# Optimization experiments

Hardware: AMD Instinct MI355X
Metric: run time of the kernel (lower is better)

Reference implementation:

```python
import jax, jax.numpy as jnp
import numpy as np

N, E, G, D, L, T = 50000, 100000, 2000, 300, 5, 10
NUM_ATOM, NUM_CHIR, NUM_BOND, NUM_DIR = 120, 3, 6, 3


def setup_inputs() -> dict:
    key = jax.random.key(0)
    ks = jax.random.split(key, 24)
    s = 1.0 / np.sqrt(D)
    inp = {
        'x': jnp.stack([jax.random.randint(ks[0], (N,), 0, NUM_ATOM),
                        jax.random.randint(ks[1], (N,), 0, NUM_CHIR)], axis=1),
        'edge_index': jax.random.randint(ks[2], (2, E), 0, N),
        'edge_attr': jnp.stack([jax.random.randint(ks[3], (E,), 0, 4),
                                jax.random.randint(ks[4], (E,), 0, NUM_DIR)], axis=1),
        'batch': jnp.sort(jax.random.randint(ks[5], (N,), 0, G)),
        'x1': jnp.stack([jax.random.randint(ks[6], (N,), 0, NUM_ATOM),
                         jax.random.randint(ks[7], (N,), 0, NUM_CHIR)], axis=1),
        'edge_index1': jax.random.randint(ks[8], (2, E), 0, N),
        'edge_attr1': jnp.stack([jax.random.randint(ks[9], (E,), 0, 4),
                                 jax.random.randint(ks[10], (E,), 0, NUM_DIR)], axis=1),
        'batch1': jnp.sort(jax.random.randint(ks[11], (N,), 0, G)),
        'xemb1': jax.random.normal(ks[12], (NUM_ATOM, D)) * s,
        'xemb2': jax.random.normal(ks[13], (NUM_CHIR, D)) * s,
        'eemb1': jax.random.normal(ks[14], (L, NUM_BOND, D)) * s,
        'eemb2': jax.random.normal(ks[15], (L, NUM_DIR, D)) * s,
        'W1': jax.random.normal(ks[16], (L, D, 2 * D)) * s,
        'b1': jnp.zeros((L, 2 * D)),
        'W2': jax.random.normal(ks[17], (L, 2 * D, D)) * (1.0 / np.sqrt(2 * D)),
        'b2': jnp.zeros((L, D)),
        'gamma': jnp.ones((L, D)),
        'beta': jnp.zeros((L, D)),
        'predW': jax.random.normal(ks[18], (D, T)) * s,
        'predb': jnp.zeros((T,)),
    }
    return inp


def _gnn(xi, ei, ea, xemb1, xemb2, eemb1, eemb2, W1, b1, W2, b2, gamma, beta):
    n = xi.shape[0]
    h = xemb1[xi[:, 0]] + xemb2[xi[:, 1]]  # [N, D]
    loop = jnp.arange(n)
    src = jnp.concatenate([ei[0], loop])
    dst = jnp.concatenate([ei[1], loop])
    # self-loop edge attr = [4, 0]
    sl = jnp.concatenate([jnp.full((n, 1), 4, ea.dtype), jnp.zeros((n, 1), ea.dtype)], axis=1)
    eaf = jnp.concatenate([ea, sl], axis=0)
    for l in range(L):
        eemb = eemb1[l][eaf[:, 0]] + eemb2[l][eaf[:, 1]]     # [E+N, D]
        msg = h[src] + eemb                                   # gather
        agg = jax.ops.segment_sum(msg, dst, num_segments=n)   # scatter-add
        h2 = jax.nn.relu(agg @ W1[l] + b1[l]) @ W2[l] + b2[l] # GIN MLP
        mu = h2.mean(axis=0)
        var = ((h2 - mu) ** 2).mean(axis=0)                   # batchnorm (train stats)
        h2 = gamma[l] * (h2 - mu) * jax.lax.rsqrt(var + 1e-5) + beta[l]
        if l < L - 1:
            h2 = jax.nn.relu(h2)
        h = h2
    return h  # JK='last'


def _mean_pool(node_rep, batch):
    s = jax.ops.segment_sum(node_rep, batch, num_segments=G)
    cnt = jax.ops.segment_sum(jnp.ones((node_rep.shape[0],), node_rep.dtype), batch, num_segments=G)
    return s / jnp.maximum(cnt, 1.0)[:, None]


def reference(x, edge_index, edge_attr, batch, x1, edge_index1, edge_attr1, batch1,
              xemb1, xemb2, eemb1, eemb2, W1, b1, W2, b2, gamma, beta, predW, predb):
    node_rep = _gnn(x, edge_index, edge_attr, xemb1, xemb2, eemb1, eemb2, W1, b1, W2, b2, gamma, beta)
    node_rep1 = _gnn(x1, edge_index1, edge_attr1, xemb1, xemb2, eemb1, eemb2, W1, b1, W2, b2, gamma, beta)
    graph_rep = _mean_pool(node_rep, batch)
    graph_rep1 = _mean_pool(node_rep1, batch1)
    pred = graph_rep @ predW + predb
    pred1 = graph_rep1 @ predW + predb
    return (pred, graph_rep, node_rep, pred1, graph_rep1, node_rep1)
```

## Files before the change

kernel.cpp:

```cpp
#include <hip/hip_runtime.h>
#include <hip/hip_bf16.h>

typedef unsigned short ushort_t;
typedef short v8s __attribute__((ext_vector_type(8)));
typedef unsigned short v8u __attribute__((ext_vector_type(8)));
typedef unsigned short v4u __attribute__((ext_vector_type(4)));
typedef float v4f __attribute__((ext_vector_type(4)));

#define N_NODES 50000
#define N_EDGES 100000
#define N_GRAPH 2000
#define DIM     300
#define DIM2    600
#define NLAYER  5
#define NTASK   10
#define D4      75
#define D4P     80

#define LDA  304
#define NPAD 50048
#define KST1 10
#define KST2 19

#define KB1 40
#define NT1 5
#define KB2 76
#define NT2 3
#define MT_TILES 391

#define AS1 __attribute__((address_space(1)))
#define AS3 __attribute__((address_space(3)))
static __device__ __forceinline__ void gload_lds16(const void* g, void* l) {
    __builtin_amdgcn_global_load_lds((AS1 void*)(g), (AS3 void*)(l), 16, 0, 0);
}

static __device__ __forceinline__ ushort_t f2bf(float f) {
    unsigned int u;
    __builtin_memcpy(&u, &f, 4);
    unsigned int lsb = (u >> 16) & 1u;
    u += 0x7fffu + lsb;
    return (ushort_t)(u >> 16);
}
static __device__ __forceinline__ void split2(float f, ushort_t& h, ushort_t& l) {
    unsigned int u;
    __builtin_memcpy(&u, &f, 4);
    h = (ushort_t)(u >> 16);
    unsigned int um = u & 0xFFFF0000u;
    float hf;
    __builtin_memcpy(&hf, &um, 4);
    float lf = f - hf;
    unsigned int ul;
    __builtin_memcpy(&ul, &lf, 4);
    l = (ushort_t)(ul >> 16);
}

static __device__ __forceinline__ int swz_wgid(int orig, int nwg) {
    int xcd = orig & 7;
    int seq = orig >> 3;
    int q = nwg >> 3, r = nwg & 7;
    int base = (xcd < r) ? xcd * (q + 1) : r * (q + 1) + (xcd - r) * q;
    return base + seq;
}

__global__ void k_embed_init(const int* __restrict__ x,
                             const float* __restrict__ xe1,
                             const float* __restrict__ xe2,
                             float* __restrict__ h) {
    int tid = blockIdx.x * blockDim.x + threadIdx.x;
    if (tid >= N_NODES * D4) return;
    int node = tid / D4;
    int d0 = (tid % D4) * 4;
    int i0 = x[node * 2 + 0];
    int i1 = x[node * 2 + 1];
    float4 a = *(const float4*)(xe1 + (size_t)i0 * DIM + d0);
    float4 b = *(const float4*)(xe2 + (size_t)i1 * DIM + d0);
    float4 o;
    o.x = a.x + b.x; o.y = a.y + b.y; o.z = a.z + b.z; o.w = a.w + b.w;
    *(float4*)(h + (size_t)node * LDA + d0) = o;
}

__global__ void k_deg(const int* __restrict__ ei, int* __restrict__ deg) {
    int e = blockIdx.x * blockDim.x + threadIdx.x;
    if (e >= N_EDGES) return;
    atomicAdd(&deg[ei[N_EDGES + e]], 1);
}

__global__ void k_scan1(const int* __restrict__ deg, int* __restrict__ excl,
                        int* __restrict__ blksum) {
    __shared__ int s[256];
    int i = blockIdx.x * 256 + threadIdx.x;
    int v = (i < N_NODES) ? deg[i] : 0;
    s[threadIdx.x] = v;
    __syncthreads();
#pragma unroll
    for (int o = 1; o < 256; o <<= 1) {
        int t = (threadIdx.x >= o) ? s[threadIdx.x - o] : 0;
        __syncthreads();
        s[threadIdx.x] += t;
        __syncthreads();
    }
    if (i < N_NODES) excl[i] = s[threadIdx.x] - v;
    if (threadIdx.x == 255) blksum[blockIdx.x] = s[255];
}

__global__ void k_scan2(int* __restrict__ blksum, int* __restrict__ blkoff, int nblk) {
    __shared__ int s[256];
    int v = (threadIdx.x < nblk) ? blksum[threadIdx.x] : 0;
    s[threadIdx.x] = v;
    __syncthreads();
#pragma unroll
    for (int o = 1; o < 256; o <<= 1) {
        int t = (threadIdx.x >= o) ? s[threadIdx.x - o] : 0;
        __syncthreads();
        s[threadIdx.x] += t;
        __syncthreads();
    }
    if (threadIdx.x < nblk) blkoff[threadIdx.x] = s[threadIdx.x] - v;
}

__global__ void k_scan3(const int* __restrict__ excl, const int* __restrict__ blkoff,
                        int* __restrict__ rowptr, int* __restrict__ fillptr) {
    int i = blockIdx.x * blockDim.x + threadIdx.x;
    if (i > N_NODES) return;
    int v = (i < N_NODES) ? (excl[i] + blkoff[i >> 8]) : N_EDGES;
    rowptr[i] = v;
    if (i < N_NODES) fillptr[i] = v;
}

__global__ void k_fill(const int* __restrict__ ei, const int* __restrict__ ea,
                       int* __restrict__ fillptr,
                       int* __restrict__ csrc, int* __restrict__ cea) {
    int e = blockIdx.x * blockDim.x + threadIdx.x;
    if (e >= N_EDGES) return;
    int dst = ei[N_EDGES + e];
    int pos = atomicAdd(&fillptr[dst], 1);
    csrc[pos] = ei[e];
    cea[pos] = (ea[2 * e + 0] << 16) | ea[2 * e + 1];
}

template <bool BN>
__global__ void k_gather_agg(const int* __restrict__ rowptr,
                             const int* __restrict__ csrc,
                             const int* __restrict__ cea,
                             const float* __restrict__ hin,
                             const float* __restrict__ ee1,
                             const float* __restrict__ ee2,
                             const float* __restrict__ ee1sl,
                             const float* __restrict__ ee2sl,
                             const float* __restrict__ bnmean,
                             const float* __restrict__ bnrstd,
                             const float* __restrict__ bngam,
                             const float* __restrict__ bnbet,
                             ushort_t* __restrict__ aghi,
                             ushort_t* __restrict__ aglo) {
    int tid = blockIdx.x * blockDim.x + threadIdx.x;
    if (tid >= N_NODES * D4P) return;
    int node = tid / D4P;
    int c = tid % D4P;
    int d0 = c * 4;
    const int mt = node >> 7, m = node & 127;
    const int ks = d0 >> 5, kb = (d0 >> 3) & 3, jq = d0 & 7;
    const size_t off = (((size_t)mt * KST1 + ks) * 4 + kb) * 1024 + m * 8 + jq;
    if (c >= D4) {
        v4u z = (v4u){0, 0, 0, 0};
        *(v4u*)(aghi + off) = z;
        *(v4u*)(aglo + off) = z;
        return;
    }
    float4 m4, r4, g4, b4;
    if (BN) {
        m4 = *(const float4*)(bnmean + d0);
        r4 = *(const float4*)(bnrstd + d0);
        g4 = *(const float4*)(bngam + d0);
        b4 = *(const float4*)(bnbet + d0);
    }
    auto bn4 = [&](float4 v) -> float4 {
        if (BN) {
            v.x = fmaxf((v.x - m4.x) * r4.x * g4.x + b4.x, 0.f);
            v.y = fmaxf((v.y - m4.y) * r4.y * g4.y + b4.y, 0.f);
            v.z = fmaxf((v.z - m4.z) * r4.z * g4.z + b4.z, 0.f);
            v.w = fmaxf((v.w - m4.w) * r4.w * g4.w + b4.w, 0.f);
        }
        return v;
    };
    float4 a = bn4(*(const float4*)(hin + (size_t)node * LDA + d0));
    float4 e1 = *(const float4*)(ee1sl + d0);
    float4 e2 = *(const float4*)(ee2sl + d0);
    a.x += e1.x + e2.x; a.y += e1.y + e2.y; a.z += e1.z + e2.z; a.w += e1.w + e2.w;
    int p0 = rowptr[node], p1 = rowptr[node + 1];
    for (int p = p0; p < p1; ++p) {
        int src = csrc[p];
        int pk = cea[p];
        int a0 = pk >> 16, a1 = pk & 0xFFFF;
        float4 hv = bn4(*(const float4*)(hin + (size_t)src * LDA + d0));
        float4 f1 = *(const float4*)(ee1 + (size_t)a0 * DIM + d0);
        float4 f2 = *(const float4*)(ee2 + (size_t)a1 * DIM + d0);
        a.x += hv.x + f1.x + f2.x;
        a.y += hv.y + f1.y + f2.y;
        a.z += hv.z + f1.z + f2.z;
        a.w += hv.w + f1.w + f2.w;
    }
    float av[4] = {a.x, a.y, a.z, a.w};
    v4u hh, ll;
#pragma unroll
    for (int i = 0; i < 4; ++i) {
        ushort_t uh, ul;
        split2(av[i], uh, ul);
        hh[i] = uh;
        ll[i] = ul;
    }
    *(v4u*)(aghi + off) = hh;
    *(v4u*)(aglo + off) = ll;
}

__global__ void k_pack_w(const float* __restrict__ W,
                         ushort_t* __restrict__ hi,
                         ushort_t* __restrict__ lo,
                         int K, int N, int KBv, int NTv, int total) {
    int idx = blockIdx.x * blockDim.x + threadIdx.x;
    if (idx >= total) return;
    int j = idx & 7;
    int n = (idx >> 3) & 127;
    int tmp = idx >> 10;
    int kb = tmp % KBv; tmp /= KBv;
    int nt = tmp % NTv;
    int l = tmp / NTv;
    int k = kb * 8 + j;
    int ng = nt * 128 + n;
    float v = 0.f;
    if (k < K && ng < N) v = W[((size_t)l * K + k) * N + ng];
    ushort_t h, lw;
    split2(v, h, lw);
    hi[idx] = h;
    lo[idx] = lw;
}

template <bool RELU, bool SPLITA, bool BNSTAT, typename OT>
__global__ __launch_bounds__(256) void k_gemm_mfma(
        const ushort_t* __restrict__ Ahi,
        const ushort_t* __restrict__ Alo,
        const ushort_t* __restrict__ Bhi,
        const ushort_t* __restrict__ Blo,
        const float* __restrict__ bias,
        OT* __restrict__ C,
        double* __restrict__ bnsum,
        double* __restrict__ bnsq,
        int M, int N, int Ksteps, int KBv, int NTv, int nwg,
        int ldc, int ncap, int ksout) {
    alignas(16) __shared__ ushort_t sBhi[8192];
    alignas(16) __shared__ ushort_t sBlo[8192];

    const int wgid = swz_wgid(blockIdx.x, nwg);
    const int nt = wgid % NTv;
    const int mt = wgid / NTv;
    const int t = threadIdx.x;

    const int w = t >> 6;
    const int lane = t & 63;
    const int wm = w >> 1;
    const int wn = w & 1;
    const int quad = lane >> 4;
    const int lr = lane & 15;

    v4f acc[4][4];
#pragma unroll
    for (int i = 0; i < 4; ++i)
#pragma unroll
        for (int j = 0; j < 4; ++j) acc[i][j] = (v4f){0.f, 0.f, 0.f, 0.f};

    const int aoff = quad * 1024 + (wm * 64 + lr) * 8;

    auto stageB = [&](int buf, int ks) {
        const int bo = buf * 4096;
        const size_t bbase = ((size_t)nt * KBv + ks * 4) * 1024;
#pragma unroll
        for (int p = 0; p < 2; ++p) {
            int o = p * 2048 + t * 8;
            gload_lds16(Bhi + bbase + o, &sBhi[bo + o]);
            gload_lds16(Blo + bbase + o, &sBlo[bo + o]);
        }
    };

    stageB(0, 0);
    __syncthreads();
    int cur = 0;
    for (int ks = 0; ks < Ksteps; ++ks) {
        const ushort_t* ah = Ahi + ((size_t)mt * Ksteps + ks) * 4096 + aoff;
        const ushort_t* al = SPLITA ? (Alo + ((size_t)mt * Ksteps + ks) * 4096 + aoff) : nullptr;
        v8s a_hi[4], a_lo[4];
#pragma unroll
        for (int s = 0; s < 4; ++s) {
            a_hi[s] = *(const v8s*)(ah + s * 128);
            if (SPLITA) a_lo[s] = *(const v8s*)(al + s * 128);
        }
        __builtin_amdgcn_sched_barrier(0);
        if (ks + 1 < Ksteps) stageB(cur ^ 1, ks + 1);
        const int bo = cur * 4096;
#pragma unroll
        for (int sj = 0; sj < 4; ++sj) {
            v8s bh = *(const v8s*)&sBhi[bo + quad * 1024 + (wn * 64 + sj * 16 + lr) * 8];
            v8s bl = *(const v8s*)&sBlo[bo + quad * 1024 + (wn * 64 + sj * 16 + lr) * 8];
#pragma unroll
            for (int si = 0; si < 4; ++si) {
                acc[si][sj] = __builtin_amdgcn_mfma_f32_16x16x32_bf16(
                    a_hi[si], bh, acc[si][sj], 0, 0, 0);
                acc[si][sj] = __builtin_amdgcn_mfma_f32_16x16x32_bf16(
                    a_hi[si], bl, acc[si][sj], 0, 0, 0);
                if (SPLITA)
                    acc[si][sj] = __builtin_amdgcn_mfma_f32_16x16x32_bf16(
                        a_lo[si], bh, acc[si][sj], 0, 0, 0);
            }
        }
        __syncthreads();
        cur ^= 1;
    }

    float bsum[4], bsq[4];
    if (BNSTAT) {
#pragma unroll
        for (int sj = 0; sj < 4; ++sj) { bsum[sj] = 0.f; bsq[sj] = 0.f; }
    }
#pragma unroll
    for (int sj = 0; sj < 4; ++sj) {
        int col = nt * 128 + wn * 64 + sj * 16 + lr;
        if (col >= ncap) continue;
        float bv = (col < N) ? bias[col] : 0.f;
        size_t yb = 0;
        if (sizeof(OT) == 2)
            yb = (((size_t)mt * ksout + (col >> 5)) * 4 + ((col >> 3) & 3)) * 1024 + (col & 7);
#pragma unroll
        for (int si = 0; si < 4; ++si) {
#pragma unroll
            for (int r = 0; r < 4; ++r) {
                int m = wm * 64 + si * 16 + quad * 4 + r;
                size_t row = (size_t)mt * 128 + m;
                float v = acc[si][sj][r] + bv;
                if (RELU) v = fmaxf(v, 0.f);
                if (BNSTAT && row < (size_t)M) { bsum[sj] += v; bsq[sj] += v * v; }
                if (sizeof(OT) == 2)
                    ((ushort_t*)C)[yb + m * 8] = f2bf(v);
                else
                    ((float*)C)[row * ldc + col] = v;
            }
        }
    }
    if (BNSTAT) {
        float* sred = (float*)sBhi;
#pragma unroll
        for (int sj = 0; sj < 4; ++sj) {
            bsum[sj] += __shfl_xor(bsum[sj], 16);
            bsum[sj] += __shfl_xor(bsum[sj], 32);
            bsq[sj]  += __shfl_xor(bsq[sj], 16);
            bsq[sj]  += __shfl_xor(bsq[sj], 32);
        }
        if (quad == 0) {
#pragma unroll
            for (int sj = 0; sj < 4; ++sj) {
                int idx = wm * 128 + wn * 64 + sj * 16 + lr;
                sred[idx] = bsum[sj];
                sred[256 + idx] = bsq[sj];
            }
        }
        __syncthreads();
        if (t < 128) {
            float s = sred[t] + sred[128 + t];
            float q = sred[256 + t] + sred[256 + 128 + t];
            int col = nt * 128 + t;
            if (col < N) {
                atomicAdd(&bnsum[col], (double)s);
                atomicAdd(&bnsq[col], (double)q);
            }
        }
    }
}

__global__ void k_bn_finalize(double* __restrict__ sum,
                              double* __restrict__ sumsq,
                              float* __restrict__ mean,
                              float* __restrict__ rstd) {
    int d = threadIdx.x;
    if (d >= DIM) return;
    double mu = sum[d] / (double)N_NODES;
    double var = sumsq[d] / (double)N_NODES - mu * mu;
    if (var < 0.0) var = 0.0;
    mean[d] = (float)mu;
    rstd[d] = (float)(1.0 / sqrt(var + 1e-5));
    sum[d] = 0.0;
    sumsq[d] = 0.0;
}

__global__ __launch_bounds__(256) void k_bn_pool(const float* __restrict__ h2,
                                                 const int* __restrict__ batch,
                                                 const float* __restrict__ mean,
                                                 const float* __restrict__ rstd,
                                                 const float* __restrict__ gam,
                                                 const float* __restrict__ bet,
                                                 float* __restrict__ nodeout,
                                                 float* __restrict__ pool,
                                                 float* __restrict__ gout) {
    __shared__ float4 s[3][D4];
    const int g = blockIdx.x;
    int lo = 0, hi = N_NODES;
    while (lo < hi) {
        int m = (lo + hi) >> 1;
        if (batch[m] < g) lo = m + 1; else hi = m;
    }
    const int p0 = lo;
    hi = N_NODES;
    while (lo < hi) {
        int m = (lo + hi) >> 1;
        if (batch[m] < g + 1) lo = m + 1; else hi = m;
    }
    const int p1 = lo;

    const int t = threadIdx.x;
    if (t < 3 * D4) {
        const int c = t % D4;
        const int rc = t / D4;
        const int d0 = c * 4;
        float4 m4 = *(const float4*)(mean + d0);
        float4 r4 = *(const float4*)(rstd + d0);
        float4 g4 = *(const float4*)(gam + d0);
        float4 b4 = *(const float4*)(bet + d0);
        float4 acc = {0.f, 0.f, 0.f, 0.f};
        for (int r = p0 + rc; r < p1; r += 3) {
            float4 v = *(const float4*)(h2 + (size_t)r * LDA + d0);
            v.x = (v.x - m4.x) * r4.x * g4.x + b4.x;
            v.y = (v.y - m4.y) * r4.y * g4.y + b4.y;
            v.z = (v.z - m4.z) * r4.z * g4.z + b4.z;
            v.w = (v.w - m4.w) * r4.w * g4.w + b4.w;
            *(float4*)(nodeout + (size_t)r * DIM + d0) = v;
            acc.x += v.x; acc.y += v.y; acc.z += v.z; acc.w += v.w;
        }
        s[rc][c] = acc;
    }
    __syncthreads();
    if (t < D4) {
        float4 a = s[0][t], b = s[1][t], c = s[2][t];
        const float inv = 1.0f / fmaxf((float)(p1 - p0), 1.0f);
        float4 r;
        r.x = (a.x + b.x + c.x) * inv;
        r.y = (a.y + b.y + c.y) * inv;
        r.z = (a.z + b.z + c.z) * inv;
        r.w = (a.w + b.w + c.w) * inv;
        *(float4*)(pool + (size_t)g * DIM + t * 4) = r;
        *(float4*)(gout + (size_t)g * DIM + t * 4) = r;
    }
}

__global__ void k_pred(const float* __restrict__ pool,
                       const float* __restrict__ predW,
                       const float* __restrict__ predb,
                       float* __restrict__ out) {
    int tid = blockIdx.x * blockDim.x + threadIdx.x;
    if (tid >= N_GRAPH * NTASK) return;
    int g = tid / NTASK;
    int tt = tid % NTASK;
    float s = predb[tt];
    const float* pr = pool + (size_t)g * DIM;
    for (int k = 0; k < DIM; ++k) s += pr[k] * predW[k * NTASK + tt];
    out[(size_t)g * NTASK + tt] = s;
}

static inline int cdiv(long long a, long long b) { return (int)((a + b - 1) / b); }

extern "C" void kernel_launch(void* const* d_in, const int* in_sizes, int n_in,
                              void* d_out, int out_size, void* d_ws, size_t ws_size,
                              hipStream_t stream) {
    const int* x    = (const int*)d_in[0];
    const int* ei   = (const int*)d_in[1];
    const int* ea   = (const int*)d_in[2];
    const int* bat  = (const int*)d_in[3];
    const int* x1   = (const int*)d_in[4];
    const int* ei1  = (const int*)d_in[5];
    const int* ea1  = (const int*)d_in[6];
    const int* bat1 = (const int*)d_in[7];
    const float* xemb1 = (const float*)d_in[8];
    const float* xemb2 = (const float*)d_in[9];
    const float* eemb1 = (const float*)d_in[10];
    const float* eemb2 = (const float*)d_in[11];
    const float* W1    = (const float*)d_in[12];
    const float* b1    = (const float*)d_in[13];
    const float* W2    = (const float*)d_in[14];
    const float* b2    = (const float*)d_in[15];
    const float* gamma = (const float*)d_in[16];
    const float* beta  = (const float*)d_in[17];
    const float* predW = (const float*)d_in[18];
    const float* predb = (const float*)d_in[19];
    float* out = (float*)d_out;

    char* ws = (char*)d_ws;
    size_t off = 0;
    auto take = [&](size_t bytes) -> char* {
        char* p = ws + off;
        off += (bytes + 255) & ~(size_t)255;
        return p;
    };
    const size_t PLANE = (size_t)MT_TILES * KST1 * 4096;
    const size_t BUFSZ = PLANE * 2 * 2;
    char* bufA = take(BUFSZ);
    char* bufB = take(BUFSZ);
    float* pool   = (float*)take((size_t)N_GRAPH * DIM * 4);
    double* bnsum = (double*)take(DIM * 8 * 2);
    double* bnsq  = bnsum + DIM;
    float* bnmean = (float*)take(DIM * 4 * 2);
    float* bnrstd = bnmean + DIM;
    const size_t W1P = (size_t)NLAYER * NT1 * KB1 * 1024;
    const size_t W2P = (size_t)NLAYER * NT2 * KB2 * 1024;
    ushort_t* w1hi = (ushort_t*)take(W1P * 2);
    ushort_t* w1lo = (ushort_t*)take(W1P * 2);
    ushort_t* w2hi = (ushort_t*)take(W2P * 2);
    ushort_t* w2lo = (ushort_t*)take(W2P * 2);
    int* deg     = (int*)take(N_NODES * 4);
    int* excl    = (int*)take(N_NODES * 4);
    int* blksum  = (int*)take(256 * 4);
    int* blkoff  = (int*)take(256 * 4);
    int* fillptr = (int*)take(N_NODES * 4);
    int* rowptr0 = (int*)take((N_NODES + 1) * 4);
    int* csrc0   = (int*)take(N_EDGES * 4);
    int* cea0    = (int*)take(N_EDGES * 4);
    int* rowptr1 = (int*)take((N_NODES + 1) * 4);
    int* csrc1   = (int*)take(N_EDGES * 4);
    int* cea1    = (int*)take(N_EDGES * 4);
    (void)ws_size; (void)in_sizes; (void)n_in; (void)out_size;

    const int TB = 256;
    const int gN75 = cdiv((long long)N_NODES * D4, TB);
    const int gN80 = cdiv((long long)N_NODES * D4P, TB);
    const int gE   = cdiv(N_EDGES, TB);
    const int gScan = cdiv(N_NODES, TB);
    const int gScan3 = cdiv(N_NODES + 1, TB);
    const int NWG1 = NT1 * MT_TILES;
    const int NWG2 = NT2 * MT_TILES;

    k_pack_w<<<cdiv((long long)W1P, TB), TB, 0, stream>>>(W1, w1hi, w1lo, DIM, DIM2, KB1, NT1, (int)W1P);
    k_pack_w<<<cdiv((long long)W2P, TB), TB, 0, stream>>>(W2, w2hi, w2lo, DIM2, DIM, KB2, NT2, (int)W2P);

    auto build_csr = [&](const int* eip, const int* eap, int* rowptr, int* csrc, int* cea) {
        hipMemsetAsync(deg, 0, N_NODES * 4, stream);
        k_deg<<<gE, TB, 0, stream>>>(eip, deg);
        k_scan1<<<gScan, TB, 0, stream>>>(deg, excl, blksum);
        k_scan2<<<1, 256, 0, stream>>>(blksum, blkoff, gScan);
        k_scan3<<<gScan3, TB, 0, stream>>>(excl, blkoff, rowptr, fillptr);
        k_fill<<<gE, TB, 0, stream>>>(eip, eap, fillptr, csrc, cea);
    };
    build_csr(ei, ea, rowptr0, csrc0, cea0);
    build_csr(ei1, ea1, rowptr1, csrc1, cea1);

    hipMemsetAsync(bnsum, 0, DIM * 8 * 2, stream);

    auto run_gnn = [&](const int* xp, const int* batp,
                       const int* rowptr, const int* csrc, const int* cea,
                       float* out_pred, float* out_graph, float* out_node) {
        k_embed_init<<<gN75, TB, 0, stream>>>(xp, xemb1, xemb2, (float*)bufA);
        for (int l = 0; l < NLAYER; ++l) {
            char* pb = (l & 1) ? bufA : bufB;
            char* yb = (l & 1) ? bufB : bufA;
            ushort_t* aghi = (ushort_t*)pb;
            ushort_t* aglo = aghi + PLANE;
            const float* gin = (const float*)yb;
            ushort_t* yv = (ushort_t*)yb;
            float* h2v = (float*)pb;
            const float* ee1l = eemb1 + (size_t)l * 6 * DIM;
            const float* ee2l = eemb2 + (size_t)l * 3 * DIM;
            if (l == 0)
                k_gather_agg<false><<<gN80, TB, 0, stream>>>(
                    rowptr, csrc, cea, gin, ee1l, ee2l, ee1l + 4 * DIM, ee2l,
                    nullptr, nullptr, nullptr, nullptr, aghi, aglo);
            else
                k_gather_agg<true><<<gN80, TB, 0, stream>>>(
                    rowptr, csrc, cea, gin, ee1l, ee2l, ee1l + 4 * DIM, ee2l,
                    bnmean, bnrstd, gamma + (size_t)(l - 1) * DIM, beta + (size_t)(l - 1) * DIM,
                    aghi, aglo);
            k_gemm_mfma<true, true, false, ushort_t>
                <<<NWG1, TB, 0, stream>>>(
                    aghi, aglo,
                    w1hi + (size_t)l * NT1 * KB1 * 1024, w1lo + (size_t)l * NT1 * KB1 * 1024,
                    b1 + (size_t)l * DIM2, yv, nullptr, nullptr,
                    N_NODES, DIM2, KST1, KB1, NT1, NWG1, 0, 608, KST2);
            k_gemm_mfma<false, false, true, float>
                <<<NWG2, TB, 0, stream>>>(
                    yv, yv,
                    w2hi + (size_t)l * NT2 * KB2 * 1024, w2lo + (size_t)l * NT2 * KB2 * 1024,
                    b2 + (size_t)l * DIM, h2v, bnsum, bnsq,
                    N_NODES, DIM, KST2, KB2, NT2, NWG2, LDA, 304, 0);
            k_bn_finalize<<<1, 512, 0, stream>>>(bnsum, bnsq, bnmean, bnrstd);
        }
        k_bn_pool<<<N_GRAPH, TB, 0, stream>>>(
            (const float*)bufB, batp, bnmean, bnrstd,
            gamma + (size_t)(NLAYER - 1) * DIM, beta + (size_t)(NLAYER - 1) * DIM,
            out_node, pool, out_graph);
        k_pred<<<cdiv((long long)N_GRAPH * NTASK, TB), TB, 0, stream>>>(pool, predW, predb, out_pred);
    };

    const size_t GT = (size_t)N_GRAPH * NTASK;
    const size_t GD = (size_t)N_GRAPH * DIM;
    const size_t ND = (size_t)N_NODES * DIM;
    run_gnn(x, bat, rowptr0, csrc0, cea0, out, out + GT, out + GT + GD);
    run_gnn(x1, bat1, rowptr1, csrc1, cea1,
            out + GT + GD + ND, out + 2 * GT + GD + ND, out + 2 * GT + 2 * GD + ND);
}
```

Measured before the change: 2.004 ms.

## Batch both GNN passes into single launches and fuse embedding into first gather

The two independent graph passes are stacked along the row dimension, so each gather, GEMM, BN-finalize, pool and predict kernel runs once over both graphs instead of twice. Buffers grow to two padded halves, and BN statistics are kept per graph via a tile-half offset. The separate embedding-init kernel is removed, and layer-0 gather now looks up atom embeddings directly. This halves kernel launches and doubles the grid size for better GPU fill, at the cost of a larger workspace and per-thread graph selection branches.

```diff
diff --git a/kernel.cpp b/kernel.cpp
--- a/kernel.cpp
+++ b/kernel.cpp
@@ -27,6 +27,7 @@
 #define KB2 76
 #define NT2 3
 #define MT_TILES 391
+#define MT2      782
 
 #define AS1 __attribute__((address_space(1)))
 #define AS3 __attribute__((address_space(3)))
@@ -62,23 +63,6 @@
     return base + seq;
 }
 
-__global__ void k_embed_init(const int* __restrict__ x,
-                             const float* __restrict__ xe1,
-                             const float* __restrict__ xe2,
-                             float* __restrict__ h) {
-    int tid = blockIdx.x * blockDim.x + threadIdx.x;
-    if (tid >= N_NODES * D4) return;
-    int node = tid / D4;
-    int d0 = (tid % D4) * 4;
-    int i0 = x[node * 2 + 0];
-    int i1 = x[node * 2 + 1];
-    float4 a = *(const float4*)(xe1 + (size_t)i0 * DIM + d0);
-    float4 b = *(const float4*)(xe2 + (size_t)i1 * DIM + d0);
-    float4 o;
-    o.x = a.x + b.x; o.y = a.y + b.y; o.z = a.z + b.z; o.w = a.w + b.w;
-    *(float4*)(h + (size_t)node * LDA + d0) = o;
-}
-
 __global__ void k_deg(const int* __restrict__ ei, int* __restrict__ deg) {
     int e = blockIdx.x * blockDim.x + threadIdx.x;
     if (e >= N_EDGES) return;
@@ -138,10 +122,17 @@
     cea[pos] = (ea[2 * e + 0] << 16) | ea[2 * e + 1];
 }
 
-template <bool BN>
-__global__ void k_gather_agg(const int* __restrict__ rowptr,
-                             const int* __restrict__ csrc,
-                             const int* __restrict__ cea,
+template <bool EMB>
+__global__ void k_gather_agg(const int* __restrict__ rowptr0,
+                             const int* __restrict__ csrc0,
+                             const int* __restrict__ cea0,
+                             const int* __restrict__ rowptr1,
+                             const int* __restrict__ csrc1,
+                             const int* __restrict__ cea1,
+                             const int* __restrict__ x0,
+                             const int* __restrict__ x1,
+                             const float* __restrict__ xe1,
+                             const float* __restrict__ xe2,
                              const float* __restrict__ hin,
                              const float* __restrict__ ee1,
                              const float* __restrict__ ee2,
@@ -154,11 +145,14 @@
                              ushort_t* __restrict__ aghi,
                              ushort_t* __restrict__ aglo) {
     int tid = blockIdx.x * blockDim.x + threadIdx.x;
-    if (tid >= N_NODES * D4P) return;
-    int node = tid / D4P;
+    if (tid >= 2 * N_NODES * D4P) return;
+    int gi = tid / D4P;
     int c = tid % D4P;
+    int graph = (gi >= N_NODES) ? 1 : 0;
+    int ln = gi - graph * N_NODES;
+    int row = graph * NPAD + ln;
     int d0 = c * 4;
-    const int mt = node >> 7, m = node & 127;
+    const int mt = row >> 7, m = row & 127;
     const int ks = d0 >> 5, kb = (d0 >> 3) & 3, jq = d0 & 7;
     const size_t off = (((size_t)mt * KST1 + ks) * 4 + kb) * 1024 + m * 8 + jq;
     if (c >= D4) {
@@ -167,32 +161,47 @@
         *(v4u*)(aglo + off) = z;
         return;
     }
+    const int* rowptr = graph ? rowptr1 : rowptr0;
+    const int* csrc   = graph ? csrc1   : csrc0;
+    const int* cea    = graph ? cea1    : cea0;
+    const int* xp     = graph ? x1      : x0;
+
     float4 m4, r4, g4, b4;
-    if (BN) {
-        m4 = *(const float4*)(bnmean + d0);
-        r4 = *(const float4*)(bnrstd + d0);
+    if (!EMB) {
+        const int bo = graph * DIM + d0;
+        m4 = *(const float4*)(bnmean + bo);
+        r4 = *(const float4*)(bnrstd + bo);
         g4 = *(const float4*)(bngam + d0);
         b4 = *(const float4*)(bnbet + d0);
     }
-    auto bn4 = [&](float4 v) -> float4 {
-        if (BN) {
+    auto hval = [&](int node) -> float4 {
+        if (EMB) {
+            int i0 = xp[node * 2 + 0];
+            int i1 = xp[node * 2 + 1];
+            float4 a = *(const float4*)(xe1 + (size_t)i0 * DIM + d0);
+            float4 b = *(const float4*)(xe2 + (size_t)i1 * DIM + d0);
+            float4 o;
+            o.x = a.x + b.x; o.y = a.y + b.y; o.z = a.z + b.z; o.w = a.w + b.w;
+            return o;
+        } else {
+            float4 v = *(const float4*)(hin + (size_t)(graph * NPAD + node) * LDA + d0);
             v.x = fmaxf((v.x - m4.x) * r4.x * g4.x + b4.x, 0.f);
             v.y = fmaxf((v.y - m4.y) * r4.y * g4.y + b4.y, 0.f);
             v.z = fmaxf((v.z - m4.z) * r4.z * g4.z + b4.z, 0.f);
             v.w = fmaxf((v.w - m4.w) * r4.w * g4.w + b4.w, 0.f);
-        }
-        return v;
+            return v;
+        }
     };
-    float4 a = bn4(*(const float4*)(hin + (size_t)node * LDA + d0));
+    float4 a = hval(ln);
     float4 e1 = *(const float4*)(ee1sl + d0);
     float4 e2 = *(const float4*)(ee2sl + d0);
     a.x += e1.x + e2.x; a.y += e1.y + e2.y; a.z += e1.z + e2.z; a.w += e1.w + e2.w;
-    int p0 = rowptr[node], p1 = rowptr[node + 1];
+    int p0 = rowptr[ln], p1 = rowptr[ln + 1];
     for (int p = p0; p < p1; ++p) {
         int src = csrc[p];
         int pk = cea[p];
         int a0 = pk >> 16, a1 = pk & 0xFFFF;
-        float4 hv = bn4(*(const float4*)(hin + (size_t)src * LDA + d0));
+        float4 hv = hval(src);
         float4 f1 = *(const float4*)(ee1 + (size_t)a0 * DIM + d0);
         float4 f2 = *(const float4*)(ee2 + (size_t)a1 * DIM + d0);
         a.x += hv.x + f1.x + f2.x;
@@ -246,7 +255,7 @@
         double* __restrict__ bnsum,
         double* __restrict__ bnsq,
         int M, int N, int Ksteps, int KBv, int NTv, int nwg,
-        int ldc, int ncap, int ksout) {
+        int ldc, int ncap, int ksout, int mtHalf) {
     alignas(16) __shared__ ushort_t sBhi[8192];
     alignas(16) __shared__ ushort_t sBlo[8192];
 
@@ -315,6 +324,7 @@
         cur ^= 1;
     }
 
+    const int graph = (mt >= mtHalf) ? 1 : 0;
     float bsum[4], bsq[4];
     if (BNSTAT) {
 #pragma unroll
@@ -336,7 +346,10 @@
                 size_t row = (size_t)mt * 128 + m;
                 float v = acc[si][sj][r] + bv;
                 if (RELU) v = fmaxf(v, 0.f);
-                if (BNSTAT && row < (size_t)M) { bsum[sj] += v; bsq[sj] += v * v; }
+                if (BNSTAT) {
+                    int lrow = (mt - graph * mtHalf) * 128 + m;
+                    if (lrow < M) { bsum[sj] += v; bsq[sj] += v * v; }
+                }
                 if (sizeof(OT) == 2)
                     ((ushort_t*)C)[yb + m * 8] = f2bf(v);
                 else
@@ -367,8 +380,8 @@
             float q = sred[256 + t] + sred[256 + 128 + t];
             int col = nt * 128 + t;
             if (col < N) {
-                atomicAdd(&bnsum[col], (double)s);
-                atomicAdd(&bnsq[col], (double)q);
+                atomicAdd(&bnsum[graph * N + col], (double)s);
+                atomicAdd(&bnsq[graph * N + col], (double)q);
             }
         }
     }
@@ -378,8 +391,8 @@
                               double* __restrict__ sumsq,
                               float* __restrict__ mean,
                               float* __restrict__ rstd) {
-    int d = threadIdx.x;
-    if (d >= DIM) return;
+    int d = blockIdx.x * blockDim.x + threadIdx.x;
+    if (d >= 2 * DIM) return;
     double mu = sum[d] / (double)N_NODES;
     double var = sumsq[d] / (double)N_NODES - mu * mu;
     if (var < 0.0) var = 0.0;
@@ -390,16 +403,26 @@
 }
 
 __global__ __launch_bounds__(256) void k_bn_pool(const float* __restrict__ h2,
-                                                 const int* __restrict__ batch,
+                                                 const int* __restrict__ bat0,
+                                                 const int* __restrict__ bat1,
                                                  const float* __restrict__ mean,
                                                  const float* __restrict__ rstd,
                                                  const float* __restrict__ gam,
                                                  const float* __restrict__ bet,
-                                                 float* __restrict__ nodeout,
+                                                 float* __restrict__ node0,
+                                                 float* __restrict__ node1,
                                                  float* __restrict__ pool,
-                                                 float* __restrict__ gout) {
+                                                 float* __restrict__ gout0,
+                                                 float* __restrict__ gout1) {
     __shared__ float4 s[3][D4];
-    const int g = blockIdx.x;
+    const int bid = blockIdx.x;
+    const int graph = (bid >= N_GRAPH) ? 1 : 0;
+    const int g = bid - graph * N_GRAPH;
+    const int* batch = graph ? bat1 : bat0;
+    const float* h2g = h2 + (size_t)graph * NPAD * LDA;
+    float* nodeout = graph ? node1 : node0;
+    float* gout = graph ? gout1 : gout0;
+
     int lo = 0, hi = N_NODES;
     while (lo < hi) {
         int m = (lo + hi) >> 1;
@@ -418,13 +441,13 @@
         const int c = t % D4;
         const int rc = t / D4;
         const int d0 = c * 4;
-        float4 m4 = *(const float4*)(mean + d0);
-        float4 r4 = *(const float4*)(rstd + d0);
+        float4 m4 = *(const float4*)(mean + graph * DIM + d0);
+        float4 r4 = *(const float4*)(rstd + graph * DIM + d0);
         float4 g4 = *(const float4*)(gam + d0);
         float4 b4 = *(const float4*)(bet + d0);
         float4 acc = {0.f, 0.f, 0.f, 0.f};
         for (int r = p0 + rc; r < p1; r += 3) {
-            float4 v = *(const float4*)(h2 + (size_t)r * LDA + d0);
+            float4 v = *(const float4*)(h2g + (size_t)r * LDA + d0);
             v.x = (v.x - m4.x) * r4.x * g4.x + b4.x;
             v.y = (v.y - m4.y) * r4.y * g4.y + b4.y;
             v.z = (v.z - m4.z) * r4.z * g4.z + b4.z;
@@ -443,7 +466,7 @@
         r.y = (a.y + b.y + c.y) * inv;
         r.z = (a.z + b.z + c.z) * inv;
         r.w = (a.w + b.w + c.w) * inv;
-        *(float4*)(pool + (size_t)g * DIM + t * 4) = r;
+        *(float4*)(pool + (size_t)bid * DIM + t * 4) = r;
         *(float4*)(gout + (size_t)g * DIM + t * 4) = r;
     }
 }
@@ -451,15 +474,19 @@
 __global__ void k_pred(const float* __restrict__ pool,
                        const float* __restrict__ predW,
                        const float* __restrict__ predb,
-                       float* __restrict__ out) {
+                       float* __restrict__ out0,
+                       float* __restrict__ out1) {
     int tid = blockIdx.x * blockDim.x + threadIdx.x;
-    if (tid >= N_GRAPH * NTASK) return;
-    int g = tid / NTASK;
+    if (tid >= 2 * N_GRAPH * NTASK) return;
+    int gg = tid / NTASK;
     int tt = tid % NTASK;
+    int graph = (gg >= N_GRAPH) ? 1 : 0;
+    int g = gg - graph * N_GRAPH;
     float s = predb[tt];
-    const float* pr = pool + (size_t)g * DIM;
+    const float* pr = pool + (size_t)gg * DIM;
     for (int k = 0; k < DIM; ++k) s += pr[k] * predW[k * NTASK + tt];
-    out[(size_t)g * NTASK + tt] = s;
+    float* outp = graph ? out1 : out0;
+    outp[(size_t)g * NTASK + tt] = s;
 }
 
 static inline int cdiv(long long a, long long b) { return (int)((a + b - 1) / b); }
@@ -496,15 +523,15 @@
         off += (bytes + 255) & ~(size_t)255;
         return p;
     };
-    const size_t PLANE = (size_t)MT_TILES * KST1 * 4096;
+    const size_t PLANE = (size_t)MT2 * KST1 * 4096;
     const size_t BUFSZ = PLANE * 2 * 2;
     char* bufA = take(BUFSZ);
     char* bufB = take(BUFSZ);
-    float* pool   = (float*)take((size_t)N_GRAPH * DIM * 4);
-    double* bnsum = (double*)take(DIM * 8 * 2);
-    double* bnsq  = bnsum + DIM;
-    float* bnmean = (float*)take(DIM * 4 * 2);
-    float* bnrstd = bnmean + DIM;
+    float* pool   = (float*)take((size_t)2 * N_GRAPH * DIM * 4);
+    double* bnsum = (double*)take(2 * DIM * 8 * 2);
+    double* bnsq  = bnsum + 2 * DIM;
+    float* bnmean = (float*)take(2 * DIM * 4 * 2);
+    float* bnrstd = bnmean + 2 * DIM;
     const size_t W1P = (size_t)NLAYER * NT1 * KB1 * 1024;
     const size_t W2P = (size_t)NLAYER * NT2 * KB2 * 1024;
     ushort_t* w1hi = (ushort_t*)take(W1P * 2);
@@ -525,13 +552,12 @@
     (void)ws_size; (void)in_sizes; (void)n_in; (void)out_size;
 
     const int TB = 256;
-    const int gN75 = cdiv((long long)N_NODES * D4, TB);
-    const int gN80 = cdiv((long long)N_NODES * D4P, TB);
     const int gE   = cdiv(N_EDGES, TB);
     const int gScan = cdiv(N_NODES, TB);
     const int gScan3 = cdiv(N_NODES + 1, TB);
-    const int NWG1 = NT1 * MT_TILES;
-    const int NWG2 = NT2 * MT_TILES;
+    const int gGath = cdiv((long long)2 * N_NODES * D4P, TB);
+    const int NWG1 = NT1 * MT2;
+    const int NWG2 = NT2 * MT2;
 
     k_pack_w<<<cdiv((long long)W1P, TB), TB, 0, stream>>>(W1, w1hi, w1lo, DIM, DIM2, KB1, NT1, (int)W1P);
     k_pack_w<<<cdiv((long long)W2P, TB), TB, 0, stream>>>(W2, w2hi, w2lo, DIM2, DIM, KB2, NT2, (int)W2P);
@@ -547,56 +573,57 @@
     build_csr(ei, ea, rowptr0, csrc0, cea0);
     build_csr(ei1, ea1, rowptr1, csrc1, cea1);
 
-    hipMemsetAsync(bnsum, 0, DIM * 8 * 2, stream);
-
-    auto run_gnn = [&](const int* xp, const int* batp,
-                       const int* rowptr, const int* csrc, const int* cea,
-                       float* out_pred, float* out_graph, float* out_node) {
-        k_embed_init<<<gN75, TB, 0, stream>>>(xp, xemb1, xemb2, (float*)bufA);
-        for (int l = 0; l < NLAYER; ++l) {
-            char* pb = (l & 1) ? bufA : bufB;
-            char* yb = (l & 1) ? bufB : bufA;
-            ushort_t* aghi = (ushort_t*)pb;
-            ushort_t* aglo = aghi + PLANE;
-            const float* gin = (const float*)yb;
-            ushort_t* yv = (ushort_t*)yb;
-            float* h2v = (float*)pb;
-            const float* ee1l = eemb1 + (size_t)l * 6 * DIM;
-            const float* ee2l = eemb2 + (size_t)l * 3 * DIM;
-            if (l == 0)
-                k_gather_agg<false><<<gN80, TB, 0, stream>>>(
-                    rowptr, csrc, cea, gin, ee1l, ee2l, ee1l + 4 * DIM, ee2l,
-                    nullptr, nullptr, nullptr, nullptr, aghi, aglo);
-            else
-                k_gather_agg<true><<<gN80, TB, 0, stream>>>(
-                    rowptr, csrc, cea, gin, ee1l, ee2l, ee1l + 4 * DIM, ee2l,
-                    bnmean, bnrstd, gamma + (size_t)(l - 1) * DIM, beta + (size_t)(l - 1) * DIM,
-                    aghi, aglo);
-            k_gemm_mfma<true, true, false, ushort_t>
-                <<<NWG1, TB, 0, stream>>>(
-                    aghi, aglo,
-                    w1hi + (size_t)l * NT1 * KB1 * 1024, w1lo + (size_t)l * NT1 * KB1 * 1024,
-                    b1 + (size_t)l * DIM2, yv, nullptr, nullptr,
-                    N_NODES, DIM2, KST1, KB1, NT1, NWG1, 0, 608, KST2);
-            k_gemm_mfma<false, false, true, float>
-                <<<NWG2, TB, 0, stream>>>(
-                    yv, yv,
-                    w2hi + (size_t)l * NT2 * KB2 * 1024, w2lo + (size_t)l * NT2 * KB2 * 1024,
-                    b2 + (size_t)l * DIM, h2v, bnsum, bnsq,
-                    N_NODES, DIM, KST2, KB2, NT2, NWG2, LDA, 304, 0);
-            k_bn_finalize<<<1, 512, 0, stream>>>(bnsum, bnsq, bnmean, bnrstd);
-        }
-        k_bn_pool<<<N_GRAPH, TB, 0, stream>>>(
-            (const float*)bufB, batp, bnmean, bnrstd,
-            gamma + (size_t)(NLAYER - 1) * DIM, beta + (size_t)(NLAYER - 1) * DIM,
-            out_node, pool, out_graph);
-        k_pred<<<cdiv((long long)N_GRAPH * NTASK, TB), TB, 0, stream>>>(pool, predW, predb, out_pred);
-    };
+    hipMemsetAsync(bnsum, 0, 2 * DIM * 8 * 2, stream);
 
     const size_t GT = (size_t)N_GRAPH * NTASK;
     const size_t GD = (size_t)N_GRAPH * DIM;
     const size_t ND = (size_t)N_NODES * DIM;
-    run_gnn(x, bat, rowptr0, csrc0, cea0, out, out + GT, out + GT + GD);
-    run_gnn(x1, bat1, rowptr1, csrc1, cea1,
-            out + GT + GD + ND, out + 2 * GT + GD + ND, out + 2 * GT + 2 * GD + ND);
-}
+    float* out_pred0  = out;
+    float* out_graph0 = out + GT;
+    float* out_node0  = out + GT + GD;
+    float* out_pred1  = out + GT + GD + ND;
+    float* out_graph1 = out + 2 * GT + GD + ND;
+    float* out_node1  = out + 2 * GT + 2 * GD + ND;
+
+    for (int l = 0; l < NLAYER; ++l) {
+        char* pb = (l & 1) ? bufA : bufB;
+        char* yb = (l & 1) ? bufB : bufA;
+        ushort_t* aghi = (ushort_t*)pb;
+        ushort_t* aglo = aghi + PLANE;
+        const float* gin = (const float*)yb;
+        ushort_t* yv = (ushort_t*)yb;
+        float* h2v = (float*)pb;
+        const float* ee1l = eemb1 + (size_t)l * 6 * DIM;
+        const float* ee2l = eemb2 + (size_t)l * 3 * DIM;
+        if (l == 0)
+            k_gather_agg<true><<<gGath, TB, 0, stream>>>(
+                rowptr0, csrc0, cea0, rowptr1, csrc1, cea1, x, x1, xemb1, xemb2,
+                nullptr, ee1l, ee2l, ee1l + 4 * DIM, ee2l,
+                nullptr, nullptr, nullptr, nullptr, aghi, aglo);
+        else
+            k_gather_agg<false><<<gGath, TB, 0, stream>>>(
+                rowptr0, csrc0, cea0, rowptr1, csrc1, cea1, x, x1, xemb1, xemb2,
+                gin, ee1l, ee2l, ee1l + 4 * DIM, ee2l,
+                bnmean, bnrstd, gamma + (size_t)(l - 1) * DIM, beta + (size_t)(l - 1) * DIM,
+                aghi, aglo);
+        k_gemm_mfma<true, true, false, ushort_t>
+            <<<NWG1, TB, 0, stream>>>(
+                aghi, aglo,
+                w1hi + (size_t)l * NT1 * KB1 * 1024, w1lo + (size_t)l * NT1 * KB1 * 1024,
+                b1 + (size_t)l * DIM2, yv, nullptr, nullptr,
+                N_NODES, DIM2, KST1, KB1, NT1, NWG1, 0, 608, KST2, MT_TILES);
+        k_gemm_mfma<false, false, true, float>
+            <<<NWG2, TB, 0, stream>>>(
+                yv, yv,
+                w2hi + (size_t)l * NT2 * KB2 * 1024, w2lo + (size_t)l * NT2 * KB2 * 1024,
+                b2 + (size_t)l * DIM, h2v, bnsum, bnsq,
+                N_NODES, DIM, KST2, KB2, NT2, NWG2, LDA, 304, 0, MT_TILES);
+        k_bn_finalize<<<3, 256, 0, stream>>>(bnsum, bnsq, bnmean, bnrstd);
+    }
+    k_bn_pool<<<2 * N_GRAPH, TB, 0, stream>>>(
+        (const float*)bufB, bat, bat1, bnmean, bnrstd,
+        gamma + (size_t)(NLAYER - 1) * DIM, beta + (size_t)(NLAYER - 1) * DIM,
+        out_node0, out_node1, pool, out_graph0, out_graph1);
+    k_pred<<<cdiv((long long)2 * N_GRAPH * NTASK, TB), TB, 0, stream>>>(
+        pool, predW, predb, out_pred0, out_pred1);
+}
```

Result: no change. 1.976 ms (-1.4%).
